# Optimization experiments

Hardware: AMD Instinct MI355X
Metric: run time of the kernel (lower is better)

## Reference

```python
import jax, jax.numpy as jnp
import numpy as np

NEG_INF = -1e18  # fp32 masking constant used by the original module


def setup_inputs() -> dict:
    key0 = jax.random.key(0)
    kq, kk, kv, km, ke = jax.random.split(key0, 5)
    B, L, H, C = 2, 2048, 16, 64
    query = jax.random.normal(kq, (B, L, H, C), dtype=jnp.float32)
    key = jax.random.normal(kk, (B, L, H, C), dtype=jnp.float32)
    value = jax.random.normal(kv, (B, L, H, C), dtype=jnp.float32)
    mask = jax.random.randint(km, (B, L, L), 0, 2).astype(jnp.bool_)
    edge_scores = jax.random.normal(ke, (1, H, L, L), dtype=jnp.float32)
    return {"query": query, "key": key, "value": value, "mask": mask,
            "edge_scores": edge_scores}


def _masked_softmax(att_score, mask):
    # mask: True -> keep, False -> masked. Fill with -1e18 (fp32 path),
    # softmax, then multiply by mask (post-softmax zeroing), as in original.
    s = jnp.where(mask, att_score, NEG_INF)
    w = jax.nn.softmax(s, axis=-1)
    return w * mask.astype(w.dtype)


def reference(query, key, value, mask, edge_scores):
    # layout 'NTK': query/key/value (B, L, H, C); mask (B, Lq, Lm)
    scale = jnp.sqrt(jnp.asarray(query.shape[-1], dtype=query.dtype))
    # scores: (B, H, Lq, Lm)
    scores = jnp.einsum('binc,bjnc->bnij', query, key)
    scores = scores + edge_scores
    attn_weights = _masked_softmax(scores / scale, mask[:, None, :, :])
    # dropout rate is 0.0 -> identity
    # context: (B, Lq, H, Cv) -> (B, Lq, H*Cv)
    context = jnp.einsum('bnij,bjnc->binc', attn_weights, value)
    B, Lq = context.shape[0], context.shape[1]
    context_vec = context.reshape(B, Lq, -1)
    return (context_vec, scores, attn_weights)
```

## Files before the change

### kernel.cpp

```cpp
#include <hip/hip_runtime.h>


typedef __attribute__((ext_vector_type(8))) short bf16x8;
typedef __attribute__((ext_vector_type(4))) float f32x4;
typedef __attribute__((ext_vector_type(4))) int   i32x4;

#define LQ 2048
#define NH 16
#define CD 64
#define NHC (NH*CD)

__device__ inline short f2bf(float x) {
    union { float f; unsigned u; } v; v.f = x;
    unsigned r = v.u + 0x7FFFu + ((v.u >> 16) & 1u);
    return (short)(r >> 16);
}

__device__ inline bf16x8 pack8(f32x4 a, f32x4 b) {
    bf16x8 r;
    r[0] = f2bf(a[0]); r[1] = f2bf(a[1]); r[2] = f2bf(a[2]); r[3] = f2bf(a[3]);
    r[4] = f2bf(b[0]); r[5] = f2bf(b[1]); r[6] = f2bf(b[2]); r[7] = f2bf(b[3]);
    return r;
}

__global__ __launch_bounds__(256)
void k_prep(const float* __restrict__ kk, const float* __restrict__ v,
            short* __restrict__ Kb, short* __restrict__ Vt)
{
    const int bz = blockIdx.x >> 5;
    const int j0 = (blockIdx.x & 31) * 64;
    const int b = bz & 1, h = bz >> 1;
    const int tid = threadIdx.x;

    const int r = tid >> 2, seg = (tid & 3) * 16;
    const size_t kidx = ((size_t)((b * LQ + j0 + r) * NH + h)) * CD + seg;
    #pragma unroll
    for (int u = 0; u < 4; ++u) {
        f32x4 g = *(const f32x4*)(kk + kidx + u * 4);
        *(short4*)(Kb + kidx + u * 4) =
            make_short4(f2bf(g[0]), f2bf(g[1]), f2bf(g[2]), f2bf(g[3]));
    }

    const int rgrp = tid >> 4, c4 = tid & 15;
    const float* vp = v + ((size_t)((b * LQ + j0 + rgrp * 4) * NH + h)) * CD + c4 * 4;
    f32x4 va0 = *(const f32x4*)vp;
    f32x4 va1 = *(const f32x4*)(vp + NHC);
    f32x4 va2 = *(const f32x4*)(vp + 2 * NHC);
    f32x4 va3 = *(const f32x4*)(vp + 3 * NHC);
    #pragma unroll
    for (int cs = 0; cs < 4; ++cs) {
        *(short4*)(Vt + ((size_t)((b * NH + h) * CD + c4 * 4 + cs)) * LQ + j0 + rgrp * 4) =
            make_short4(f2bf(va0[cs]), f2bf(va1[cs]), f2bf(va2[cs]), f2bf(va3[cs]));
    }
}

__global__ __launch_bounds__(256, 4)
void k_A(const float* __restrict__ q, const short* __restrict__ Kb,
         const float* __restrict__ edge, const int* __restrict__ mask,
         float* __restrict__ sc, float* __restrict__ invout)
{
    const int flat = blockIdx.x;
    const int L = (flat & 7) * 128 + (flat >> 3);
    const int z = L >> 5;
    const int i0 = (L & 31) * 64;
    const int b = z & 1, h = z >> 1;

    const int tid = threadIdx.x;
    const int wave = tid >> 6, lane = tid & 63;
    const int quad = lane >> 4, mm = lane & 15;
    const int gi = i0 + wave * 16 + mm;

    const float* qp = q + ((size_t)((b * LQ + gi) * NH + h)) * CD;
    bf16x8 qa0 = pack8(*(const f32x4*)(qp + quad * 8), *(const f32x4*)(qp + quad * 8 + 4));
    bf16x8 qa1 = pack8(*(const f32x4*)(qp + 32 + quad * 8), *(const f32x4*)(qp + 32 + quad * 8 + 4));

    const float* erow = edge + ((size_t)(h * LQ + gi)) * LQ;
    const int*   mrow = mask + ((size_t)(b * LQ + gi)) * LQ;
    const size_t srow = ((size_t)((b * NH + h) * LQ + gi)) * LQ;
    const short* kfb = Kb + (size_t)b * LQ * NHC + (size_t)h * CD;

    f32x4 ev[4]; i32x4 mv[4];
    #pragma unroll
    for (int jt = 0; jt < 4; ++jt) {
        ev[jt] = *(const f32x4*)(erow + jt * 16 + quad * 4);
        mv[jt] = *(const i32x4*)(mrow + jt * 16 + quad * 4);
    }

    float lacc = 0.f;
    for (int jb = 0; jb < 32; ++jb) {
        const int j0 = jb * 64;
        f32x4 acc[4];
        #pragma unroll
        for (int jt = 0; jt < 4; ++jt) {
            const short* kr = kfb + (size_t)(j0 + jt * 16 + mm) * NHC + quad * 8;
            bf16x8 k0 = *(const bf16x8*)kr;
            bf16x8 k1 = *(const bf16x8*)(kr + 32);
            f32x4 a = {0.f, 0.f, 0.f, 0.f};
            a = __builtin_amdgcn_mfma_f32_16x16x32_bf16(k0, qa0, a, 0, 0, 0);
            a = __builtin_amdgcn_mfma_f32_16x16x32_bf16(k1, qa1, a, 0, 0, 0);
            acc[jt] = a;
        }
        #pragma unroll
        for (int jt = 0; jt < 4; ++jt) {
            f32x4 s4 = acc[jt] + ev[jt];
            *(f32x4*)(sc + srow + j0 + jt * 16 + quad * 4) = s4;
            lacc += (mv[jt][0] ? __expf(s4[0] * 0.125f) : 0.f)
                  + (mv[jt][1] ? __expf(s4[1] * 0.125f) : 0.f)
                  + (mv[jt][2] ? __expf(s4[2] * 0.125f) : 0.f)
                  + (mv[jt][3] ? __expf(s4[3] * 0.125f) : 0.f);
        }
        if (jb < 31) {
            #pragma unroll
            for (int jt = 0; jt < 4; ++jt) {
                ev[jt] = *(const f32x4*)(erow + j0 + 64 + jt * 16 + quad * 4);
                mv[jt] = *(const i32x4*)(mrow + j0 + 64 + jt * 16 + quad * 4);
            }
        }
    }

    lacc += __shfl_xor(lacc, 16, 64);
    lacc += __shfl_xor(lacc, 32, 64);
    if (quad == 0)
        invout[(size_t)(b * NH + h) * LQ + gi] = (lacc > 0.f) ? 1.f / lacc : 0.f;
}

__global__ __launch_bounds__(256, 4)
void k_B(const short* __restrict__ Vt, const int* __restrict__ mask,
         const float* __restrict__ invws, const float* __restrict__ sc,
         float* __restrict__ attn, float* __restrict__ ctx)
{
    const int flat = blockIdx.x;
    const int L = (flat & 7) * 128 + (flat >> 3);
    const int z = L >> 5;
    const int i0 = (L & 31) * 64;
    const int b = z & 1, h = z >> 1;

    const int tid = threadIdx.x;
    const int wave = tid >> 6, lane = tid & 63;
    const int quad = lane >> 4, mm = lane & 15;
    const int gi = i0 + wave * 16 + mm;

    const int*   mrow = mask + ((size_t)(b * LQ + gi)) * LQ;
    const size_t srow = ((size_t)((b * NH + h) * LQ + gi)) * LQ;
    const float  inv  = invws[(size_t)(b * NH + h) * LQ + gi];
    const short* vtb  = Vt + (size_t)(b * NH + h) * CD * LQ;

    f32x4 s0a = *(const f32x4*)(sc + srow + quad * 8);
    f32x4 s0b = *(const f32x4*)(sc + srow + quad * 8 + 4);
    f32x4 s1a = *(const f32x4*)(sc + srow + 32 + quad * 8);
    f32x4 s1b = *(const f32x4*)(sc + srow + 32 + quad * 8 + 4);
    i32x4 m0a = *(const i32x4*)(mrow + quad * 8);
    i32x4 m0b = *(const i32x4*)(mrow + quad * 8 + 4);
    i32x4 m1a = *(const i32x4*)(mrow + 32 + quad * 8);
    i32x4 m1b = *(const i32x4*)(mrow + 32 + quad * 8 + 4);

    f32x4 cacc[4] = { {0,0,0,0}, {0,0,0,0}, {0,0,0,0}, {0,0,0,0} };

    for (int jb = 0; jb < 32; ++jb) {
        const int j0 = jb * 64;
        f32x4 wa, wb2;
        wa[0] = m0a[0] ? __expf(s0a[0] * 0.125f) * inv : 0.f;
        wa[1] = m0a[1] ? __expf(s0a[1] * 0.125f) * inv : 0.f;
        wa[2] = m0a[2] ? __expf(s0a[2] * 0.125f) * inv : 0.f;
        wa[3] = m0a[3] ? __expf(s0a[3] * 0.125f) * inv : 0.f;
        wb2[0] = m0b[0] ? __expf(s0b[0] * 0.125f) * inv : 0.f;
        wb2[1] = m0b[1] ? __expf(s0b[1] * 0.125f) * inv : 0.f;
        wb2[2] = m0b[2] ? __expf(s0b[2] * 0.125f) * inv : 0.f;
        wb2[3] = m0b[3] ? __expf(s0b[3] * 0.125f) * inv : 0.f;
        *(f32x4*)(attn + srow + j0 + quad * 8) = wa;
        *(f32x4*)(attn + srow + j0 + quad * 8 + 4) = wb2;
        bf16x8 aw0 = pack8(wa, wb2);
        wa[0] = m1a[0] ? __expf(s1a[0] * 0.125f) * inv : 0.f;
        wa[1] = m1a[1] ? __expf(s1a[1] * 0.125f) * inv : 0.f;
        wa[2] = m1a[2] ? __expf(s1a[2] * 0.125f) * inv : 0.f;
        wa[3] = m1a[3] ? __expf(s1a[3] * 0.125f) * inv : 0.f;
        wb2[0] = m1b[0] ? __expf(s1b[0] * 0.125f) * inv : 0.f;
        wb2[1] = m1b[1] ? __expf(s1b[1] * 0.125f) * inv : 0.f;
        wb2[2] = m1b[2] ? __expf(s1b[2] * 0.125f) * inv : 0.f;
        wb2[3] = m1b[3] ? __expf(s1b[3] * 0.125f) * inv : 0.f;
        *(f32x4*)(attn + srow + j0 + 32 + quad * 8) = wa;
        *(f32x4*)(attn + srow + j0 + 32 + quad * 8 + 4) = wb2;
        bf16x8 aw1 = pack8(wa, wb2);

        if (jb < 31) {
            const int jn = j0 + 64;
            s0a = *(const f32x4*)(sc + srow + jn + quad * 8);
            s0b = *(const f32x4*)(sc + srow + jn + quad * 8 + 4);
            s1a = *(const f32x4*)(sc + srow + jn + 32 + quad * 8);
            s1b = *(const f32x4*)(sc + srow + jn + 32 + quad * 8 + 4);
            m0a = *(const i32x4*)(mrow + jn + quad * 8);
            m0b = *(const i32x4*)(mrow + jn + quad * 8 + 4);
            m1a = *(const i32x4*)(mrow + jn + 32 + quad * 8);
            m1b = *(const i32x4*)(mrow + jn + 32 + quad * 8 + 4);
        }

        #pragma unroll
        for (int nt = 0; nt < 4; ++nt) {
            const short* vr = vtb + (size_t)(nt * 16 + mm) * LQ + j0 + quad * 8;
            bf16x8 b0 = *(const bf16x8*)vr;
            bf16x8 b1 = *(const bf16x8*)(vr + 32);
            cacc[nt] = __builtin_amdgcn_mfma_f32_16x16x32_bf16(aw0, b0, cacc[nt], 0, 0, 0);
            cacc[nt] = __builtin_amdgcn_mfma_f32_16x16x32_bf16(aw1, b1, cacc[nt], 0, 0, 0);
        }
    }

    const int irow = i0 + wave * 16 + quad * 4;
    #pragma unroll
    for (int nt = 0; nt < 4; ++nt) {
        const int c = nt * 16 + mm;
        #pragma unroll
        for (int reg = 0; reg < 4; ++reg) {
            const int i = irow + reg;
            ctx[((size_t)(b * LQ + i)) * NHC + h * CD + c] = cacc[nt][reg];
        }
    }
}

extern "C" void kernel_launch(void* const* d_in, const int* in_sizes, int n_in,
                              void* d_out, int out_size, void* d_ws, size_t ws_size,
                              hipStream_t stream) {
    const float* q    = (const float*)d_in[0];
    const float* k    = (const float*)d_in[1];
    const float* v    = (const float*)d_in[2];
    const int*   mask = (const int*)d_in[3];
    const float* edge = (const float*)d_in[4];

    float* out = (float*)d_out;
    float* ctx = out;
    float* sc  = out + 4194304;
    float* at  = sc + 134217728;

    short* Kb  = (short*)d_ws;
    short* Vt  = (short*)d_ws + 4194304;
    float* inv = (float*)((char*)d_ws + 16777216);

    k_prep<<<dim3(1024), 256, 0, stream>>>(k, v, Kb, Vt);
    k_A   <<<dim3(1024), 256, 0, stream>>>(q, Kb, edge, mask, sc, inv);
    k_B   <<<dim3(1024), 256, 0, stream>>>(Vt, mask, inv, sc, at, ctx);
}
```

Baseline: 1.765 ms.

## Split key dimension across waves and double grid size for attention kernels

Each block now handles 32 query rows instead of 64, with pairs of waves splitting the 2048 key columns in halves. The partial softmax sums and context accumulators are combined through shared memory after a barrier. The grid grows from 1024 to 2048 blocks and launch bounds now allow 8 blocks per CU, aiming for more concurrent waves to hide memory latency on this bandwidth-bound workload. The cost is extra shared-memory reductions and block-wide syncs, and each K/V tile is now reused by fewer query rows.

```diff
diff --git a/kernel.cpp b/kernel.cpp
--- a/kernel.cpp
+++ b/kernel.cpp
@@ -54,30 +54,34 @@
     }
 }
 
-__global__ __launch_bounds__(256, 4)
+__global__ __launch_bounds__(256, 8)
 void k_A(const float* __restrict__ q, const short* __restrict__ Kb,
          const float* __restrict__ edge, const int* __restrict__ mask,
          float* __restrict__ sc, float* __restrict__ invout)
 {
+    __shared__ float lred[2][2][16];
+
     const int flat = blockIdx.x;
-    const int L = (flat & 7) * 128 + (flat >> 3);
-    const int z = L >> 5;
-    const int i0 = (L & 31) * 64;
+    const int L = (flat & 7) * 256 + (flat >> 3);
+    const int z = L >> 6;
+    const int i0 = (L & 63) * 32;
     const int b = z & 1, h = z >> 1;
 
     const int tid = threadIdx.x;
     const int wave = tid >> 6, lane = tid & 63;
     const int quad = lane >> 4, mm = lane & 15;
-    const int gi = i0 + wave * 16 + mm;
+    const int rg = wave >> 1, jh = wave & 1;
+    const int gi = i0 + rg * 16 + mm;
+    const int jbase = jh * 1024;
 
     const float* qp = q + ((size_t)((b * LQ + gi) * NH + h)) * CD;
     bf16x8 qa0 = pack8(*(const f32x4*)(qp + quad * 8), *(const f32x4*)(qp + quad * 8 + 4));
     bf16x8 qa1 = pack8(*(const f32x4*)(qp + 32 + quad * 8), *(const f32x4*)(qp + 32 + quad * 8 + 4));
 
-    const float* erow = edge + ((size_t)(h * LQ + gi)) * LQ;
-    const int*   mrow = mask + ((size_t)(b * LQ + gi)) * LQ;
-    const size_t srow = ((size_t)((b * NH + h) * LQ + gi)) * LQ;
-    const short* kfb = Kb + (size_t)b * LQ * NHC + (size_t)h * CD;
+    const float* erow = edge + ((size_t)(h * LQ + gi)) * LQ + jbase;
+    const int*   mrow = mask + ((size_t)(b * LQ + gi)) * LQ + jbase;
+    const size_t srow = ((size_t)((b * NH + h) * LQ + gi)) * LQ + jbase;
+    const short* kfb = Kb + (size_t)b * LQ * NHC + (size_t)h * CD + (size_t)jbase * NHC;
 
     f32x4 ev[4]; i32x4 mv[4];
     #pragma unroll
@@ -87,7 +91,7 @@
     }
 
     float lacc = 0.f;
-    for (int jb = 0; jb < 32; ++jb) {
+    for (int jb = 0; jb < 16; ++jb) {
         const int j0 = jb * 64;
         f32x4 acc[4];
         #pragma unroll
@@ -109,7 +113,7 @@
                   + (mv[jt][2] ? __expf(s4[2] * 0.125f) : 0.f)
                   + (mv[jt][3] ? __expf(s4[3] * 0.125f) : 0.f);
         }
-        if (jb < 31) {
+        if (jb < 15) {
             #pragma unroll
             for (int jt = 0; jt < 4; ++jt) {
                 ev[jt] = *(const f32x4*)(erow + j0 + 64 + jt * 16 + quad * 4);
@@ -120,30 +124,38 @@
 
     lacc += __shfl_xor(lacc, 16, 64);
     lacc += __shfl_xor(lacc, 32, 64);
-    if (quad == 0)
-        invout[(size_t)(b * NH + h) * LQ + gi] = (lacc > 0.f) ? 1.f / lacc : 0.f;
-}
-
-__global__ __launch_bounds__(256, 4)
+    if (quad == 0) lred[rg][jh][mm] = lacc;
+    __syncthreads();
+    if (jh == 0 && quad == 0) {
+        const float tot = lred[rg][0][mm] + lred[rg][1][mm];
+        invout[(size_t)(b * NH + h) * LQ + gi] = (tot > 0.f) ? 1.f / tot : 0.f;
+    }
+}
+
+__global__ __launch_bounds__(256, 8)
 void k_B(const short* __restrict__ Vt, const int* __restrict__ mask,
          const float* __restrict__ invws, const float* __restrict__ sc,
          float* __restrict__ attn, float* __restrict__ ctx)
 {
+    __shared__ float red[2][16][64];
+
     const int flat = blockIdx.x;
-    const int L = (flat & 7) * 128 + (flat >> 3);
-    const int z = L >> 5;
-    const int i0 = (L & 31) * 64;
+    const int L = (flat & 7) * 256 + (flat >> 3);
+    const int z = L >> 6;
+    const int i0 = (L & 63) * 32;
     const int b = z & 1, h = z >> 1;
 
     const int tid = threadIdx.x;
     const int wave = tid >> 6, lane = tid & 63;
     const int quad = lane >> 4, mm = lane & 15;
-    const int gi = i0 + wave * 16 + mm;
-
-    const int*   mrow = mask + ((size_t)(b * LQ + gi)) * LQ;
-    const size_t srow = ((size_t)((b * NH + h) * LQ + gi)) * LQ;
+    const int rg = wave >> 1, jh = wave & 1;
+    const int gi = i0 + rg * 16 + mm;
+    const int jbase = jh * 1024;
+
+    const int*   mrow = mask + ((size_t)(b * LQ + gi)) * LQ + jbase;
+    const size_t srow = ((size_t)((b * NH + h) * LQ + gi)) * LQ + jbase;
     const float  inv  = invws[(size_t)(b * NH + h) * LQ + gi];
-    const short* vtb  = Vt + (size_t)(b * NH + h) * CD * LQ;
+    const short* vtb  = Vt + (size_t)(b * NH + h) * CD * LQ + jbase;
 
     f32x4 s0a = *(const f32x4*)(sc + srow + quad * 8);
     f32x4 s0b = *(const f32x4*)(sc + srow + quad * 8 + 4);
@@ -156,7 +168,7 @@
 
     f32x4 cacc[4] = { {0,0,0,0}, {0,0,0,0}, {0,0,0,0}, {0,0,0,0} };
 
-    for (int jb = 0; jb < 32; ++jb) {
+    for (int jb = 0; jb < 16; ++jb) {
         const int j0 = jb * 64;
         f32x4 wa, wb2;
         wa[0] = m0a[0] ? __expf(s0a[0] * 0.125f) * inv : 0.f;
@@ -182,7 +194,7 @@
         *(f32x4*)(attn + srow + j0 + 32 + quad * 8 + 4) = wb2;
         bf16x8 aw1 = pack8(wa, wb2);
 
-        if (jb < 31) {
+        if (jb < 15) {
             const int jn = j0 + 64;
             s0a = *(const f32x4*)(sc + srow + jn + quad * 8);
             s0b = *(const f32x4*)(sc + srow + jn + quad * 8 + 4);
@@ -204,14 +216,24 @@
         }
     }
 
-    const int irow = i0 + wave * 16 + quad * 4;
-    #pragma unroll
-    for (int nt = 0; nt < 4; ++nt) {
-        const int c = nt * 16 + mm;
-        #pragma unroll
-        for (int reg = 0; reg < 4; ++reg) {
-            const int i = irow + reg;
-            ctx[((size_t)(b * LQ + i)) * NHC + h * CD + c] = cacc[nt][reg];
+    if (jh == 1) {
+        #pragma unroll
+        for (int nt = 0; nt < 4; ++nt)
+            #pragma unroll
+            for (int reg = 0; reg < 4; ++reg)
+                red[rg][quad * 4 + reg][nt * 16 + mm] = cacc[nt][reg];
+    }
+    __syncthreads();
+    if (jh == 0) {
+        const int irow = i0 + rg * 16 + quad * 4;
+        #pragma unroll
+        for (int nt = 0; nt < 4; ++nt) {
+            const int c = nt * 16 + mm;
+            #pragma unroll
+            for (int reg = 0; reg < 4; ++reg) {
+                const float s = cacc[nt][reg] + red[rg][quad * 4 + reg][c];
+                ctx[((size_t)(b * LQ + irow + reg)) * NHC + h * CD + c] = s;
+            }
         }
     }
 }
@@ -235,6 +257,6 @@
     float* inv = (float*)((char*)d_ws + 16777216);
 
     k_prep<<<dim3(1024), 256, 0, stream>>>(k, v, Kb, Vt);
-    k_A   <<<dim3(1024), 256, 0, stream>>>(q, Kb, edge, mask, sc, inv);
-    k_B   <<<dim3(1024), 256, 0, stream>>>(Vt, mask, inv, sc, at, ctx);
-}
+    k_A   <<<dim3(2048), 256, 0, stream>>>(q, Kb, edge, mask, sc, inv);
+    k_B   <<<dim3(2048), 256, 0, stream>>>(Vt, mask, inv, sc, at, ctx);
+}
```

Measured after the change: 1.822 ms. 3.2% more time.
